# Kernel tuning notes

Measured on AMD Instinct MI355X. Metric: run time of the kernel, lower is better.

## Reference

```python
import jax, jax.numpy as jnp
import numpy as np

TEMPERATURE = 0.5


def setup_inputs() -> dict:
    key = jax.random.key(0)
    k1, k2 = jax.random.split(key)
    emb_i = jax.random.normal(k1, (4096, 512), dtype=jnp.float32)
    emb_j = jax.random.normal(k2, (4096, 512), dtype=jnp.float32)
    return {"emb_i": emb_i, "emb_j": emb_j}


def reference(emb_i, emb_j):
    # NT-Xent (SimCLR) loss, vectorized over the original per-sample python loop.
    N = emb_i.shape[0]
    z_i = emb_i / jnp.linalg.norm(emb_i, axis=1, keepdims=True)
    z_j = emb_j / jnp.linalg.norm(emb_j, axis=1, keepdims=True)
    z = jnp.concatenate([z_i, z_j], axis=0)  # [2N, d]
    # cosine similarity of unit vectors == dot product
    sim = z @ z.T                             # [2N, 2N]
    exp_sim = jnp.exp(sim / TEMPERATURE)
    # denominator excludes self-similarity (the scatter-zero in the original)
    denom = exp_sim.sum(axis=1) - jnp.diagonal(exp_sim)
    idx = jnp.arange(2 * N)
    pos_idx = jnp.concatenate([jnp.arange(N) + N, jnp.arange(N)])
    num = exp_sim[idx, pos_idx]               # positive-pair similarities
    loss = -jnp.log(num / denom)
    return loss.mean()
```

## Files before the change

### kernel.cpp

```cpp
#include <hip/hip_runtime.h>
#include <hip/hip_bf16.h>

typedef __attribute__((ext_vector_type(4))) int i32x4;

#define AS1 __attribute__((address_space(1)))
#define AS3 __attribute__((address_space(3)))

#define DDIM 512
#define BK 64

__global__ __launch_bounds__(256) void norm_pd_kernel(
    const float* __restrict__ ei, const float* __restrict__ ej,
    unsigned char* __restrict__ zq, float* __restrict__ pd,
    float* __restrict__ rowsum, float* __restrict__ out, int N) {
  const int k = blockIdx.x;
  const int t = threadIdx.x;
  const float2 a = *reinterpret_cast<const float2*>(ei + (size_t)k * DDIM + t * 2);
  const float2 b = *reinterpret_cast<const float2*>(ej + (size_t)k * DDIM + t * 2);
  float sii = a.x * a.x + a.y * a.y;
  float sjj = b.x * b.x + b.y * b.y;
  float sij = a.x * b.x + a.y * b.y;
#pragma unroll
  for (int off = 32; off; off >>= 1) {
    sii += __shfl_down(sii, off);
    sjj += __shfl_down(sjj, off);
    sij += __shfl_down(sij, off);
  }
  __shared__ float red[3][4];
  if ((t & 63) == 0) { red[0][t >> 6] = sii; red[1][t >> 6] = sjj; red[2][t >> 6] = sij; }
  __syncthreads();
  sii = red[0][0] + red[0][1] + red[0][2] + red[0][3];
  sjj = red[1][0] + red[1][1] + red[1][2] + red[1][3];
  sij = red[2][0] + red[2][1] + red[2][2] + red[2][3];
  const float rsi = rsqrtf(sii), rsj = rsqrtf(sjj);

  const int qa0 = (int)rintf(127.0f * a.x * rsi);
  const int qa1 = (int)rintf(127.0f * a.y * rsi);
  const int qb0 = (int)rintf(127.0f * b.x * rsj);
  const int qb1 = (int)rintf(127.0f * b.y * rsj);
  const unsigned short wa = (unsigned short)(qa0 & 0xff) | ((unsigned short)(qa1 & 0xff) << 8);
  const unsigned short wb = (unsigned short)(qb0 & 0xff) | ((unsigned short)(qb1 & 0xff) << 8);
  *reinterpret_cast<unsigned short*>(zq + (size_t)k * DDIM + t * 2) = wa;
  *reinterpret_cast<unsigned short*>(zq + (size_t)(N + k) * DDIM + t * 2) = wb;
  if (t == 0) {
    pd[k] = sij * rsi * rsj;
    rowsum[k] = 0.0f;
    rowsum[N + k] = 0.0f;
    if (k == 0) out[0] = 0.0f;
  }
}


#define MFMAI8(A, B, C) __builtin_amdgcn_mfma_i32_16x16x64_i8((A), (B), (C), 0, 0, 0)

__global__ __launch_bounds__(256, 4) void simloss_main(
    const unsigned char* __restrict__ zq, float* __restrict__ rowsum, int nwg) {
  const int orig = blockIdx.x;
  const int q = nwg >> 3, r8 = nwg & 7;
  const int xcd = orig & 7, pos0 = orig >> 3;
  const int t0 = (xcd < r8 ? xcd * (q + 1) : r8 * (q + 1) + (xcd - r8) * q) + pos0;

  const float ff = sqrtf(8.0f * (float)t0 + 1.0f);
  int by = (int)((ff - 1.0f) * 0.5f);
  while ((by + 1) * (by + 2) / 2 <= t0) ++by;
  while (by * (by + 1) / 2 > t0) --by;
  const int bx = t0 - by * (by + 1) / 2;

  const int row0 = bx * 128;
  const int col0 = by * 128;

  __shared__ unsigned char lds[3][2][8192];

  const int tid = threadIdx.x;
  const int w = tid >> 6;
  const int l = tid & 63;
  const int wr = (w >> 1) * 64;
  const int wc = (w & 1) * 64;
  const int lrow = l & 15;
  const int g = l >> 4;

  i32x4 acc[4][4] = {};

  auto stage = [&](int buf, int k0) {
#pragma unroll
    for (int half = 0; half < 2; ++half) {
      const int baserow = half ? col0 : row0;
#pragma unroll
      for (int it = 0; it < 2; ++it) {
        const int pp = it * 256 + tid;
        const int row = pp >> 2;
        const int s = pp & 3;
        const int gs = (s - (row >> 1)) & 3;
        const unsigned char* src = zq + (size_t)(baserow + row) * DDIM + k0 + gs * 16;
        char* dst = (char*)&lds[buf][half][0] + (unsigned)((it * 256 + w * 64) * 16);
        __builtin_amdgcn_global_load_lds((const AS1 void*)src, (AS3 void*)dst, 16, 0, 0);
      }
    }
  };

  auto compute = [&](int buf) {
    const unsigned char* ab = &lds[buf][0][0];
    const unsigned char* bb = &lds[buf][1][0];
    i32x4 Af[4], Bf[4];
#pragma unroll
    for (int mf = 0; mf < 4; ++mf) {
      const int rr = wr + mf * 16 + lrow;
      Af[mf] = *reinterpret_cast<const i32x4*>(ab + rr * 64 + (((g + (rr >> 1)) & 3) << 4));
    }
#pragma unroll
    for (int nf = 0; nf < 4; ++nf) {
      const int cc = wc + nf * 16 + lrow;
      Bf[nf] = *reinterpret_cast<const i32x4*>(bb + cc * 64 + (((g + (cc >> 1)) & 3) << 4));
    }
#pragma unroll
    for (int mf = 0; mf < 4; ++mf)
#pragma unroll
      for (int nf = 0; nf < 4; ++nf)
        acc[mf][nf] = MFMAI8(Af[mf], Bf[nf], acc[mf][nf]);
  };

  stage(0, 0);
  stage(1, BK);

#pragma unroll
  for (int t = 0; t < 8; ++t) {
    if (t < 6) {
      stage((t + 2) % 3, (t + 2) * BK);
      asm volatile("s_waitcnt vmcnt(8)" ::: "memory");
    } else if (t == 6) {
      asm volatile("s_waitcnt vmcnt(4)" ::: "memory");
    } else {
      asm volatile("s_waitcnt vmcnt(0)" ::: "memory");
    }
    __builtin_amdgcn_s_barrier();
    compute(t % 3);
    __builtin_amdgcn_s_barrier();
  }

  const float SC = 2.0f * 1.44269504088896340736f / 16129.0f;
  const int lgrp = l >> 4;
  const int lcol = l & 15;

  float e[4][4][4];
#pragma unroll
  for (int mf = 0; mf < 4; ++mf)
#pragma unroll
    for (int nf = 0; nf < 4; ++nf)
#pragma unroll
      for (int rg = 0; rg < 4; ++rg)
        e[mf][nf][rg] = exp2f((float)acc[mf][nf][rg] * SC);

#pragma unroll
  for (int mf = 0; mf < 4; ++mf) {
    float rs[4];
#pragma unroll
    for (int rg = 0; rg < 4; ++rg) {
      float s = 0.0f;
#pragma unroll
      for (int nf = 0; nf < 4; ++nf) s += e[mf][nf][rg];
      rs[rg] = s;
    }
#pragma unroll
    for (int off = 1; off < 16; off <<= 1) {
#pragma unroll
      for (int rg = 0; rg < 4; ++rg) rs[rg] += __shfl_xor(rs[rg], off);
    }
    if (lcol == 0) {
      const int rowb = row0 + wr + mf * 16 + lgrp * 4;
#pragma unroll
      for (int rg = 0; rg < 4; ++rg) atomicAdd(&rowsum[rowb + rg], rs[rg]);
    }
  }

  if (bx != by) {
#pragma unroll
    for (int nf = 0; nf < 4; ++nf) {
      float cs = 0.0f;
#pragma unroll
      for (int mf = 0; mf < 4; ++mf)
#pragma unroll
        for (int rg = 0; rg < 4; ++rg) cs += e[mf][nf][rg];
      cs += __shfl_xor(cs, 16);
      cs += __shfl_xor(cs, 32);
      if (lgrp == 0) atomicAdd(&rowsum[col0 + wc + nf * 16 + lcol], cs);
    }
  }
}

__global__ __launch_bounds__(1024) void finalize_kernel(
    const float* __restrict__ rowsum, const float* __restrict__ pd,
    float* __restrict__ out, int M, int N) {
  const int i = blockIdx.x * 1024 + threadIdx.x;
  const float E2 = 7.38905609893065f;
  float acc = 0.0f;
  if (i < M) {
    const float denom = rowsum[i] - E2;
    const int kk = (i < N) ? i : (i - N);
    acc = logf(denom) - 2.0f * pd[kk];
  }
#pragma unroll
  for (int off = 32; off; off >>= 1) acc += __shfl_down(acc, off);
  __shared__ float red[16];
  const int t = threadIdx.x;
  if ((t & 63) == 0) red[t >> 6] = acc;
  __syncthreads();
  if (t < 64) {
    float s = (t < 16) ? red[t] : 0.0f;
#pragma unroll
    for (int off = 8; off; off >>= 1) s += __shfl_down(s, off);
    if (t == 0) atomicAdd(out, s / (float)M);
  }
}

extern "C" void kernel_launch(void* const* d_in, const int* in_sizes, int n_in,
                              void* d_out, int out_size, void* d_ws, size_t ws_size,
                              hipStream_t stream) {
  const float* ei = (const float*)d_in[0];
  const float* ej = (const float*)d_in[1];
  float* out = (float*)d_out;

  const int N = in_sizes[0] / DDIM;
  const int M = 2 * N;
  const int NT = M / 128;
  const int NTRI = NT * (NT + 1) / 2;

  char* ws = (char*)d_ws;
  unsigned char* zq = (unsigned char*)ws;
  float* pd = (float*)(ws + (size_t)M * DDIM);
  float* rowsum = (float*)(ws + (size_t)M * DDIM + (size_t)N * 4);

  norm_pd_kernel<<<N, 256, 0, stream>>>(ei, ej, zq, pd, rowsum, out, N);
  simloss_main<<<NTRI, 256, 0, stream>>>(zq, rowsum, NTRI);
  finalize_kernel<<<(M + 1023) / 1024, 1024, 0, stream>>>(rowsum, pd, out, M, N);
}
```

Measured before the change: 47.48 us.

## Compute two row tiles per workgroup sharing one B panel in sim loss

Each workgroup now computes a 256x128 block (two A row tiles against one B column tile) instead of a single 128x128 triangle tile, so B fragments are reused across two MFMA accumulator sets. The grid is remapped to 1056 blocks covering the upper triangle, with special handling for diagonal tiles and duplicated diagonal blocks. The pipeline moves from triple to double buffering with three panels per stage, and launch bounds drop to 2 waves per SIMD to fit the doubled accumulators. The block count is hardcoded for N=4096, and lower occupancy may reduce latency hiding.

```diff
diff --git a/kernel.cpp b/kernel.cpp
--- a/kernel.cpp
+++ b/kernel.cpp
@@ -53,23 +53,34 @@
 
 #define MFMAI8(A, B, C) __builtin_amdgcn_mfma_i32_16x16x64_i8((A), (B), (C), 0, 0, 0)
 
-__global__ __launch_bounds__(256, 4) void simloss_main(
+__global__ __launch_bounds__(256, 2) void simloss_main(
     const unsigned char* __restrict__ zq, float* __restrict__ rowsum, int nwg) {
   const int orig = blockIdx.x;
   const int q = nwg >> 3, r8 = nwg & 7;
   const int xcd = orig & 7, pos0 = orig >> 3;
-  const int t0 = (xcd < r8 ? xcd * (q + 1) : r8 * (q + 1) + (xcd - r8) * q) + pos0;
-
-  const float ff = sqrtf(8.0f * (float)t0 + 1.0f);
-  int by = (int)((ff - 1.0f) * 0.5f);
-  while ((by + 1) * (by + 2) / 2 <= t0) ++by;
-  while (by * (by + 1) / 2 > t0) --by;
-  const int bx = t0 - by * (by + 1) / 2;
-
-  const int row0 = bx * 128;
-  const int col0 = by * 128;
-
-  __shared__ unsigned char lds[3][2][8192];
+  const int id = (xcd < r8 ? xcd * (q + 1) : r8 * (q + 1) + (xcd - r8) * q) + pos0;
+
+  int r0b, r1b, byb;
+  bool dup = false, t1diag = false;
+  if (id < 1024) {
+    int m = (int)sqrtf((float)id);
+    while ((m + 1) * (m + 1) <= id) ++m;
+    while (m * m > id) --m;
+    int by, p;
+    if (id < m * m + m) { by = 2 * m;     p = id - m * m; }
+    else                { by = 2 * m + 1; p = id - m * m - m; }
+    r0b = 2 * p; r1b = 2 * p + 1; byb = by;
+    t1diag = (r1b == byb);
+  } else {
+    const int s = id - 1024;
+    byb = 2 * s; r0b = byb; r1b = byb; dup = true;
+  }
+
+  const int arow0 = r0b * 128;
+  const int arow1 = r1b * 128;
+  const int bcol  = byb * 128;
+
+  __shared__ unsigned char lds[2][3][8192];
 
   const int tid = threadIdx.x;
   const int w = tid >> 6;
@@ -79,12 +90,13 @@
   const int lrow = l & 15;
   const int g = l >> 4;
 
-  i32x4 acc[4][4] = {};
+  i32x4 acc0[4][4] = {};
+  i32x4 acc1[4][4] = {};
 
   auto stage = [&](int buf, int k0) {
 #pragma unroll
-    for (int half = 0; half < 2; ++half) {
-      const int baserow = half ? col0 : row0;
+    for (int panel = 0; panel < 3; ++panel) {
+      const int baserow = (panel == 0) ? arow0 : (panel == 1 ? arow1 : bcol);
 #pragma unroll
       for (int it = 0; it < 2; ++it) {
         const int pp = it * 256 + tid;
@@ -92,20 +104,23 @@
         const int s = pp & 3;
         const int gs = (s - (row >> 1)) & 3;
         const unsigned char* src = zq + (size_t)(baserow + row) * DDIM + k0 + gs * 16;
-        char* dst = (char*)&lds[buf][half][0] + (unsigned)((it * 256 + w * 64) * 16);
+        char* dst = (char*)&lds[buf][panel][0] + (unsigned)((it * 256 + w * 64) * 16);
         __builtin_amdgcn_global_load_lds((const AS1 void*)src, (AS3 void*)dst, 16, 0, 0);
       }
     }
   };
 
   auto compute = [&](int buf) {
-    const unsigned char* ab = &lds[buf][0][0];
-    const unsigned char* bb = &lds[buf][1][0];
-    i32x4 Af[4], Bf[4];
+    const unsigned char* a0 = &lds[buf][0][0];
+    const unsigned char* a1 = &lds[buf][1][0];
+    const unsigned char* bb = &lds[buf][2][0];
+    i32x4 Af0[4], Af1[4], Bf[4];
 #pragma unroll
     for (int mf = 0; mf < 4; ++mf) {
       const int rr = wr + mf * 16 + lrow;
-      Af[mf] = *reinterpret_cast<const i32x4*>(ab + rr * 64 + (((g + (rr >> 1)) & 3) << 4));
+      const int off = rr * 64 + (((g + (rr >> 1)) & 3) << 4);
+      Af0[mf] = *reinterpret_cast<const i32x4*>(a0 + off);
+      Af1[mf] = *reinterpret_cast<const i32x4*>(a1 + off);
     }
 #pragma unroll
     for (int nf = 0; nf < 4; ++nf) {
@@ -115,25 +130,23 @@
 #pragma unroll
     for (int mf = 0; mf < 4; ++mf)
 #pragma unroll
-      for (int nf = 0; nf < 4; ++nf)
-        acc[mf][nf] = MFMAI8(Af[mf], Bf[nf], acc[mf][nf]);
+      for (int nf = 0; nf < 4; ++nf) {
+        acc0[mf][nf] = MFMAI8(Af0[mf], Bf[nf], acc0[mf][nf]);
+        acc1[mf][nf] = MFMAI8(Af1[mf], Bf[nf], acc1[mf][nf]);
+      }
   };
 
   stage(0, 0);
-  stage(1, BK);
-
 #pragma unroll
   for (int t = 0; t < 8; ++t) {
-    if (t < 6) {
-      stage((t + 2) % 3, (t + 2) * BK);
-      asm volatile("s_waitcnt vmcnt(8)" ::: "memory");
-    } else if (t == 6) {
-      asm volatile("s_waitcnt vmcnt(4)" ::: "memory");
+    if (t < 7) {
+      stage((t & 1) ^ 1, (t + 1) * BK);
+      asm volatile("s_waitcnt vmcnt(6)" ::: "memory");
     } else {
       asm volatile("s_waitcnt vmcnt(0)" ::: "memory");
     }
     __builtin_amdgcn_s_barrier();
-    compute(t % 3);
+    compute(t & 1);
     __builtin_amdgcn_s_barrier();
   }
 
@@ -141,48 +154,95 @@
   const int lgrp = l >> 4;
   const int lcol = l & 15;
 
-  float e[4][4][4];
-#pragma unroll
-  for (int mf = 0; mf < 4; ++mf)
-#pragma unroll
-    for (int nf = 0; nf < 4; ++nf)
-#pragma unroll
-      for (int rg = 0; rg < 4; ++rg)
-        e[mf][nf][rg] = exp2f((float)acc[mf][nf][rg] * SC);
-
-#pragma unroll
-  for (int mf = 0; mf < 4; ++mf) {
-    float rs[4];
-#pragma unroll
-    for (int rg = 0; rg < 4; ++rg) {
-      float s = 0.0f;
-#pragma unroll
-      for (int nf = 0; nf < 4; ++nf) s += e[mf][nf][rg];
-      rs[rg] = s;
-    }
-#pragma unroll
-    for (int off = 1; off < 16; off <<= 1) {
-#pragma unroll
-      for (int rg = 0; rg < 4; ++rg) rs[rg] += __shfl_xor(rs[rg], off);
-    }
-    if (lcol == 0) {
-      const int rowb = row0 + wr + mf * 16 + lgrp * 4;
-#pragma unroll
-      for (int rg = 0; rg < 4; ++rg) atomicAdd(&rowsum[rowb + rg], rs[rg]);
-    }
-  }
-
-  if (bx != by) {
-#pragma unroll
-    for (int nf = 0; nf < 4; ++nf) {
-      float cs = 0.0f;
-#pragma unroll
-      for (int mf = 0; mf < 4; ++mf)
-#pragma unroll
-        for (int rg = 0; rg < 4; ++rg) cs += e[mf][nf][rg];
-      cs += __shfl_xor(cs, 16);
-      cs += __shfl_xor(cs, 32);
-      if (lgrp == 0) atomicAdd(&rowsum[col0 + wc + nf * 16 + lcol], cs);
+  {
+    float e[4][4][4];
+#pragma unroll
+    for (int mf = 0; mf < 4; ++mf)
+#pragma unroll
+      for (int nf = 0; nf < 4; ++nf)
+#pragma unroll
+        for (int rg = 0; rg < 4; ++rg)
+          e[mf][nf][rg] = exp2f((float)acc0[mf][nf][rg] * SC);
+
+#pragma unroll
+    for (int mf = 0; mf < 4; ++mf) {
+      float rs[4];
+#pragma unroll
+      for (int rg = 0; rg < 4; ++rg) {
+        float s = 0.0f;
+#pragma unroll
+        for (int nf = 0; nf < 4; ++nf) s += e[mf][nf][rg];
+        rs[rg] = s;
+      }
+#pragma unroll
+      for (int off = 1; off < 16; off <<= 1) {
+#pragma unroll
+        for (int rg = 0; rg < 4; ++rg) rs[rg] += __shfl_xor(rs[rg], off);
+      }
+      if (lcol == 0) {
+        const int rowb = arow0 + wr + mf * 16 + lgrp * 4;
+#pragma unroll
+        for (int rg = 0; rg < 4; ++rg) atomicAdd(&rowsum[rowb + rg], rs[rg]);
+      }
+    }
+    if (!dup) {
+#pragma unroll
+      for (int nf = 0; nf < 4; ++nf) {
+        float cs = 0.0f;
+#pragma unroll
+        for (int mf = 0; mf < 4; ++mf)
+#pragma unroll
+          for (int rg = 0; rg < 4; ++rg) cs += e[mf][nf][rg];
+        cs += __shfl_xor(cs, 16);
+        cs += __shfl_xor(cs, 32);
+        if (lgrp == 0) atomicAdd(&rowsum[bcol + wc + nf * 16 + lcol], cs);
+      }
+    }
+  }
+
+  if (!dup) {
+    float e[4][4][4];
+#pragma unroll
+    for (int mf = 0; mf < 4; ++mf)
+#pragma unroll
+      for (int nf = 0; nf < 4; ++nf)
+#pragma unroll
+        for (int rg = 0; rg < 4; ++rg)
+          e[mf][nf][rg] = exp2f((float)acc1[mf][nf][rg] * SC);
+
+#pragma unroll
+    for (int mf = 0; mf < 4; ++mf) {
+      float rs[4];
+#pragma unroll
+      for (int rg = 0; rg < 4; ++rg) {
+        float s = 0.0f;
+#pragma unroll
+        for (int nf = 0; nf < 4; ++nf) s += e[mf][nf][rg];
+        rs[rg] = s;
+      }
+#pragma unroll
+      for (int off = 1; off < 16; off <<= 1) {
+#pragma unroll
+        for (int rg = 0; rg < 4; ++rg) rs[rg] += __shfl_xor(rs[rg], off);
+      }
+      if (lcol == 0) {
+        const int rowb = arow1 + wr + mf * 16 + lgrp * 4;
+#pragma unroll
+        for (int rg = 0; rg < 4; ++rg) atomicAdd(&rowsum[rowb + rg], rs[rg]);
+      }
+    }
+    if (!t1diag) {
+#pragma unroll
+      for (int nf = 0; nf < 4; ++nf) {
+        float cs = 0.0f;
+#pragma unroll
+        for (int mf = 0; mf < 4; ++mf)
+#pragma unroll
+          for (int rg = 0; rg < 4; ++rg) cs += e[mf][nf][rg];
+        cs += __shfl_xor(cs, 16);
+        cs += __shfl_xor(cs, 32);
+        if (lgrp == 0) atomicAdd(&rowsum[bcol + wc + nf * 16 + lcol], cs);
+      }
     }
   }
 }
@@ -221,8 +281,7 @@
 
   const int N = in_sizes[0] / DDIM;
   const int M = 2 * N;
-  const int NT = M / 128;
-  const int NTRI = NT * (NT + 1) / 2;
+  const int NBLK = 1056;
 
   char* ws = (char*)d_ws;
   unsigned char* zq = (unsigned char*)ws;
@@ -230,6 +289,6 @@
   float* rowsum = (float*)(ws + (size_t)M * DDIM + (size_t)N * 4);
 
   norm_pd_kernel<<<N, 256, 0, stream>>>(ei, ej, zq, pd, rowsum, out, N);
-  simloss_main<<<NTRI, 256, 0, stream>>>(zq, rowsum, NTRI);
+  simloss_main<<<NBLK, 256, 0, stream>>>(zq, rowsum, NBLK);
   finalize_kernel<<<(M + 1023) / 1024, 1024, 0, stream>>>(rowsum, pd, out, M, N);
 }
```

New measurement: 52.09 us. 1.1x slower.
